# Kernel tuning notes

Measured on AMD Instinct MI355X. Metric: run time of the kernel, lower is better.

The kernel has to match this reference:

```python
import jax, jax.numpy as jnp
from jax import lax
import numpy as np

EPS = 1e-5

def _layer_norm(x):
    mu = jnp.mean(x, axis=-1, keepdims=True)
    var = jnp.mean(jnp.square(x - mu), axis=-1, keepdims=True)
    return (x - mu) / jnp.sqrt(var + EPS)

def setup_inputs() -> dict:
    key = jax.random.key(0)
    k1, k2 = jax.random.split(key)
    B, S, D = 2, 2048, 128
    n_hashes, num_buckets = 8, 32
    x = jax.random.normal(k1, (B, S, D), dtype=jnp.float32)
    input_mask = jnp.ones((B, S), dtype=jnp.float32)
    # random rotations for LSH hashing: (B, D, n_hashes, num_buckets//2)
    rotations = jax.random.normal(k2, (B, D, n_hashes, num_buckets // 2), dtype=jnp.float32)
    return {"x": x, "input_mask": input_mask, "rotations": rotations, "num_buckets": num_buckets}

def reference(x, input_mask, rotations, num_buckets):
    B, S, D = x.shape
    xn = _layer_norm(x)
    # LSH hashing: rotate, concat +/-, argmax over bucket axis -> (B, n_hashes, S)
    rot = jnp.einsum('bnd,bdhk->bhnk', xn, rotations)
    rot = jnp.concatenate([rot, -rot], axis=-1)
    buckets = jnp.argmax(rot, axis=-1)
    xm = xn * input_mask[..., None]
    # source loop reassigns round_buckets each hash round; only the last survives
    round_buckets = buckets[:, -1, :]  # (B, S)
    scale = 1.0 / jnp.sqrt(jnp.asarray(D, dtype=x.dtype))
    def body(out, bucket_id):
        m = (round_buckets == bucket_id).astype(xm.dtype)[..., None]  # (B,S,1)
        cb = xm * m  # zero out tokens outside the bucket (faithful to source)
        scores = jnp.einsum('bsd,btd->bst', cb, cb) * scale  # (B,S,S)
        attn = jax.nn.softmax(scores, axis=-1)
        out = out + jnp.einsum('bst,btd->bsd', attn, cb) * m
        return out, None
    out, _ = lax.scan(body, jnp.zeros_like(xm), jnp.arange(num_buckets))
    return out
```

## Files before the change

### kernel.cpp

```cpp
#include <hip/hip_runtime.h>
#include <math.h>

constexpr int B = 2;
constexpr int S = 2048;
constexpr int D = 128;
constexpr int NH = 8;
constexpr int NK = 16;
constexpr int NB = 32;
constexpr float EPS = 1e-5f;
constexpr float SCALE = 0.08838834764831845f;

constexpr int MAXN = 192;
constexpr int KP   = 136;
constexpr int TP   = 200;
constexpr int QSPLIT = 4;

typedef __attribute__((ext_vector_type(8))) short bf16x8;
typedef __attribute__((ext_vector_type(4))) float f32x4;

__device__ __forceinline__ ushort f2bf(float f) {
    uint u = __float_as_uint(f);
    u += 0x7FFFu + ((u >> 16) & 1u);
    return (ushort)(u >> 16);
}

__global__ __launch_bounds__(256) void ln_hash_kernel(
    const float* __restrict__ x, const float* __restrict__ mask,
    const float* __restrict__ rot, ushort* __restrict__ xmb,
    int* __restrict__ bucket, float* __restrict__ selfp)
{
    const int wave = threadIdx.x >> 6;
    const int lane = threadIdx.x & 63;
    const int row  = blockIdx.x * 4 + wave;
    const int b    = row >> 11;

    const float v0 = x[(size_t)row * D + lane];
    const float v1 = x[(size_t)row * D + lane + 64];

    float s = v0 + v1;
    #pragma unroll
    for (int off = 32; off > 0; off >>= 1) s += __shfl_xor(s, off, 64);
    const float mu = s * (1.0f / 128.0f);

    const float c0 = v0 - mu, c1 = v1 - mu;
    float s2 = c0 * c0 + c1 * c1;
    #pragma unroll
    for (int off = 32; off > 0; off >>= 1) s2 += __shfl_xor(s2, off, 64);
    const float rstd = 1.0f / sqrtf(s2 * (1.0f / 128.0f) + EPS);

    const float xn0 = c0 * rstd, xn1 = c1 * rstd;
    const float mk = mask[row];
    xmb[(size_t)row * D + lane]      = f2bf(xn0 * mk);
    xmb[(size_t)row * D + lane + 64] = f2bf(xn1 * mk);

    const float* r0 = rot + (((size_t)(b * D + lane)) * NH + (NH - 1)) * NK;
    const float* r1 = rot + (((size_t)(b * D + lane + 64)) * NH + (NH - 1)) * NK;
    float racc[NK];
    #pragma unroll
    for (int k = 0; k < NK; ++k) racc[k] = xn0 * r0[k] + xn1 * r1[k];
    #pragma unroll
    for (int k = 0; k < NK; ++k) {
        float t = racc[k];
        #pragma unroll
        for (int off = 32; off > 0; off >>= 1) t += __shfl_xor(t, off, 64);
        racc[k] = t;
    }

    float best = racc[0]; int bi = 0;
    #pragma unroll
    for (int k = 1; k < NK; ++k) if (racc[k] > best) { best = racc[k]; bi = k; }
    #pragma unroll
    for (int k = 0; k < NK; ++k) if (-racc[k] > best) { best = -racc[k]; bi = k + NK; }

    if (lane == 0) {
        bucket[row] = bi;
        selfp[row] = SCALE * s2 * rstd * rstd * mk * mk;
    }
}

__global__ __launch_bounds__(256) void attn_kernel(
    const ushort* __restrict__ xmb, const int* __restrict__ bucket,
    const float* __restrict__ selfp, float* __restrict__ out)
{
    const int bg   = blockIdx.x >> 2;
    const int qs   = blockIdx.x & 3;
    const int b    = bg >> 5;
    const int beta = bg & 31;
    const int tid  = threadIdx.x;
    const int lane = tid & 63;
    const int wave = tid >> 6;
    const int col  = lane & 15;
    const int quad = lane >> 4;

    __shared__ __align__(16) ushort Kb[MAXN * KP];
    __shared__ __align__(16) ushort KTb[D * TP];
    __shared__ __align__(16) float  w[16 * TP];
    __shared__ __align__(16) ushort Pt[16 * TP];
    __shared__ int   idx[MAXN];
    __shared__ float scratch[256];
    __shared__ float Mrow[16], invrow[16];
    __shared__ int   wsum[4];

    const int base = b * S;
    const int4* bp = (const int4*)(bucket + base);
    const int4 v0 = bp[tid * 2];
    const int4 v1 = bp[tid * 2 + 1];
    int m0 = (v0.x == beta) | ((v0.y == beta) << 1) | ((v0.z == beta) << 2) |
             ((v0.w == beta) << 3) | ((v1.x == beta) << 4) | ((v1.y == beta) << 5) |
             ((v1.z == beta) << 6) | ((v1.w == beta) << 7);
    const int cntl = __popc(m0);

    int inc = cntl;
    #pragma unroll
    for (int off = 1; off < 64; off <<= 1) {
        const int t = __shfl_up(inc, off, 64);
        if (lane >= off) inc += t;
    }
    if (lane == 63) wsum[wave] = inc;
    __syncthreads();
    int start = inc - cntl;
    #pragma unroll
    for (int wv = 0; wv < 4; ++wv) if (wv < wave) start += wsum[wv];
    const int ntot = wsum[0] + wsum[1] + wsum[2] + wsum[3];
    const int n = min(ntot, MAXN);

    {
        const int t0 = tid * 8;
        int p = start;
        #pragma unroll
        for (int k = 0; k < 8; ++k)
            if ((m0 >> k) & 1) { if (p < MAXN) idx[p] = t0 + k; ++p; }
    }
    __syncthreads();
    if (n == 0) return;
    const int npad32 = (n + 31) & ~31;

    for (int c = tid; c < n * 16; c += 256) {
        const int i = c >> 4, ch = c & 15;
        *(bf16x8*)&Kb[i * KP + ch * 8] =
            *(const bf16x8*)(xmb + (size_t)(base + idx[i]) * D + ch * 8);
    }
    __syncthreads();

    for (int e = tid; e < n * D; e += 256) {
        const int j = e >> 7, d = e & 127;
        KTb[d * TP + j] = Kb[j * KP + d];
    }
    for (int e = tid; e < D * 32; e += 256) {
        const int d = e >> 5, j = n + (e & 31);
        if (j < npad32) KTb[d * TP + j] = 0;
    }
    for (int e = tid; e < 16 * 32; e += 256) {
        const int r = e >> 5, j = n + (e & 31);
        if (j < npad32) Pt[r * TP + j] = 0;
    }
    __syncthreads();

    for (int qt = qs; qt * 16 < n; qt += QSPLIT) {
        const int q0 = qt * 16;
        const int rows = min(16, n - q0);

        for (int kt = wave; kt * 16 < n; kt += 4) {
            const int J0 = kt * 16;
            f32x4 acc = {0.f, 0.f, 0.f, 0.f};
            #pragma unroll
            for (int ks = 0; ks < 4; ++ks) {
                const bf16x8 a = *(const bf16x8*)&Kb[(q0 + col) * KP + quad * 8 + ks * 32];
                const bf16x8 bb = *(const bf16x8*)&Kb[(J0 + col) * KP + quad * 8 + ks * 32];
                acc = __builtin_amdgcn_mfma_f32_16x16x32_bf16(a, bb, acc, 0, 0, 0);
            }
            #pragma unroll
            for (int r = 0; r < 4; ++r)
                w[(quad * 4 + r) * TP + J0 + col] = acc[r] * SCALE;
        }
        __syncthreads();

        if (tid < rows)
            w[tid * TP + q0 + tid] = selfp[base + idx[q0 + tid]];
        __syncthreads();

        {
            const int r = tid >> 4, g = tid & 15;
            float pm = 0.0f;
            if (r < rows)
                for (int j = g; j < n; j += 16) pm = fmaxf(pm, w[r * TP + j]);
            scratch[tid] = pm;
            __syncthreads();
            if (tid < 16 && tid < rows) {
                float m = scratch[tid * 16];
                #pragma unroll
                for (int k = 1; k < 16; ++k) m = fmaxf(m, scratch[tid * 16 + k]);
                Mrow[tid] = m;
            }
            __syncthreads();
            float ps = 0.0f;
            if (r < rows) {
                const float M = Mrow[r];
                for (int j = g; j < n; j += 16) {
                    const float e = expf(w[r * TP + j] - M);
                    Pt[r * TP + j] = f2bf(e);
                    ps += e;
                }
            }
            scratch[tid] = ps;
            __syncthreads();
            if (tid < 16 && tid < rows) {
                float ssum = 0.0f;
                #pragma unroll
                for (int k = 0; k < 16; ++k) ssum += scratch[tid * 16 + k];
                ssum += (float)(S - n) * expf(-Mrow[tid]);
                invrow[tid] = 1.0f / ssum;
            }
            __syncthreads();
        }

        for (int dt = wave; dt < 8; dt += 4) {
            f32x4 acc = {0.f, 0.f, 0.f, 0.f};
            for (int ks = 0; ks < npad32 / 32; ++ks) {
                const bf16x8 a = *(const bf16x8*)&Pt[col * TP + ks * 32 + quad * 8];
                const bf16x8 bb = *(const bf16x8*)&KTb[(dt * 16 + col) * TP + ks * 32 + quad * 8];
                acc = __builtin_amdgcn_mfma_f32_16x16x32_bf16(a, bb, acc, 0, 0, 0);
            }
            #pragma unroll
            for (int r = 0; r < 4; ++r) {
                const int rr = quad * 4 + r;
                if (rr < rows)
                    out[(size_t)(base + idx[q0 + rr]) * D + dt * 16 + col] =
                        acc[r] * invrow[rr];
            }
        }
        __syncthreads();
    }
}

extern "C" void kernel_launch(void* const* d_in, const int* in_sizes, int n_in,
                              void* d_out, int out_size, void* d_ws, size_t ws_size,
                              hipStream_t stream) {
    const float* x    = (const float*)d_in[0];
    const float* mask = (const float*)d_in[1];
    const float* rot  = (const float*)d_in[2];

    char* ws = (char*)d_ws;
    ushort* xmb  = (ushort*)ws;                  ws += (size_t)B * S * D * sizeof(ushort);
    int*    bkt  = (int*)ws;                     ws += (size_t)B * S * sizeof(int);
    float*  self = (float*)ws;
    float*  out  = (float*)d_out;

    ln_hash_kernel<<<B * S / 4, 256, 0, stream>>>(x, mask, rot, xmb, bkt, self);
    attn_kernel<<<B * NB * QSPLIT, 256, 0, stream>>>(xmb, bkt, self, out);
}
```

Baseline: 79.11 us.

## Fuse LN-hash and bucket attention into one cooperative kernel with grid sync

Merges the layernorm/hash kernel and the attention kernel into a single cooperative launch of 256 blocks, where each block first normalizes and hashes 16 rows and then a grid-wide sync precedes the bucket attention. The transpose into KTb now happens during the gather, removing a pass and a barrier. The softmax row max and sum reductions use wave shuffles instead of shared scratch and several __syncthreads. This removes one kernel launch and some barriers, at the cost of a grid barrier and less parallelism in the hashing phase.

```diff
diff --git a/kernel.cpp b/kernel.cpp
--- a/kernel.cpp
+++ b/kernel.cpp
@@ -1,5 +1,8 @@
 #include <hip/hip_runtime.h>
+#include <hip/hip_cooperative_groups.h>
 #include <math.h>
+
+namespace cg = cooperative_groups;
 
 constexpr int B = 2;
 constexpr int S = 2048;
@@ -14,6 +17,7 @@
 constexpr int KP   = 136;
 constexpr int TP   = 200;
 constexpr int QSPLIT = 4;
+constexpr int GRID  = B * NB * QSPLIT;
 
 typedef __attribute__((ext_vector_type(8))) short bf16x8;
 typedef __attribute__((ext_vector_type(4))) float f32x4;
@@ -24,82 +28,80 @@
     return (ushort)(u >> 16);
 }
 
-__global__ __launch_bounds__(256) void ln_hash_kernel(
+__global__ __launch_bounds__(256) void fused_kernel(
     const float* __restrict__ x, const float* __restrict__ mask,
     const float* __restrict__ rot, ushort* __restrict__ xmb,
-    int* __restrict__ bucket, float* __restrict__ selfp)
+    int* __restrict__ bucket, float* __restrict__ selfp,
+    float* __restrict__ out)
 {
-    const int wave = threadIdx.x >> 6;
-    const int lane = threadIdx.x & 63;
-    const int row  = blockIdx.x * 4 + wave;
-    const int b    = row >> 11;
-
-    const float v0 = x[(size_t)row * D + lane];
-    const float v1 = x[(size_t)row * D + lane + 64];
-
-    float s = v0 + v1;
-    #pragma unroll
-    for (int off = 32; off > 0; off >>= 1) s += __shfl_xor(s, off, 64);
-    const float mu = s * (1.0f / 128.0f);
-
-    const float c0 = v0 - mu, c1 = v1 - mu;
-    float s2 = c0 * c0 + c1 * c1;
-    #pragma unroll
-    for (int off = 32; off > 0; off >>= 1) s2 += __shfl_xor(s2, off, 64);
-    const float rstd = 1.0f / sqrtf(s2 * (1.0f / 128.0f) + EPS);
-
-    const float xn0 = c0 * rstd, xn1 = c1 * rstd;
-    const float mk = mask[row];
-    xmb[(size_t)row * D + lane]      = f2bf(xn0 * mk);
-    xmb[(size_t)row * D + lane + 64] = f2bf(xn1 * mk);
-
-    const float* r0 = rot + (((size_t)(b * D + lane)) * NH + (NH - 1)) * NK;
-    const float* r1 = rot + (((size_t)(b * D + lane + 64)) * NH + (NH - 1)) * NK;
-    float racc[NK];
-    #pragma unroll
-    for (int k = 0; k < NK; ++k) racc[k] = xn0 * r0[k] + xn1 * r1[k];
-    #pragma unroll
-    for (int k = 0; k < NK; ++k) {
-        float t = racc[k];
-        #pragma unroll
-        for (int off = 32; off > 0; off >>= 1) t += __shfl_xor(t, off, 64);
-        racc[k] = t;
-    }
-
-    float best = racc[0]; int bi = 0;
-    #pragma unroll
-    for (int k = 1; k < NK; ++k) if (racc[k] > best) { best = racc[k]; bi = k; }
-    #pragma unroll
-    for (int k = 0; k < NK; ++k) if (-racc[k] > best) { best = -racc[k]; bi = k + NK; }
-
-    if (lane == 0) {
-        bucket[row] = bi;
-        selfp[row] = SCALE * s2 * rstd * rstd * mk * mk;
-    }
-}
-
-__global__ __launch_bounds__(256) void attn_kernel(
-    const ushort* __restrict__ xmb, const int* __restrict__ bucket,
-    const float* __restrict__ selfp, float* __restrict__ out)
-{
-    const int bg   = blockIdx.x >> 2;
-    const int qs   = blockIdx.x & 3;
-    const int b    = bg >> 5;
-    const int beta = bg & 31;
     const int tid  = threadIdx.x;
+    const int wave = tid >> 6;
     const int lane = tid & 63;
-    const int wave = tid >> 6;
-    const int col  = lane & 15;
-    const int quad = lane >> 4;
 
     __shared__ __align__(16) ushort Kb[MAXN * KP];
     __shared__ __align__(16) ushort KTb[D * TP];
     __shared__ __align__(16) float  w[16 * TP];
     __shared__ __align__(16) ushort Pt[16 * TP];
     __shared__ int   idx[MAXN];
-    __shared__ float scratch[256];
-    __shared__ float Mrow[16], invrow[16];
+    __shared__ float invrow[16];
     __shared__ int   wsum[4];
+
+    #pragma unroll
+    for (int i = 0; i < 4; ++i) {
+        const int row = blockIdx.x * 16 + wave * 4 + i;
+        const int b   = row >> 11;
+
+        const float2 v = *(const float2*)(x + (size_t)row * D + lane * 2);
+        float s = v.x + v.y;
+        #pragma unroll
+        for (int off = 32; off > 0; off >>= 1) s += __shfl_xor(s, off, 64);
+        const float mu = s * (1.0f / 128.0f);
+
+        const float c0 = v.x - mu, c1 = v.y - mu;
+        float s2 = c0 * c0 + c1 * c1;
+        #pragma unroll
+        for (int off = 32; off > 0; off >>= 1) s2 += __shfl_xor(s2, off, 64);
+        const float rstd = 1.0f / sqrtf(s2 * (1.0f / 128.0f) + EPS);
+
+        const float xn0 = c0 * rstd, xn1 = c1 * rstd;
+        const float mk = mask[row];
+        ushort2 pk;
+        pk.x = f2bf(xn0 * mk);
+        pk.y = f2bf(xn1 * mk);
+        *(ushort2*)(xmb + (size_t)row * D + lane * 2) = pk;
+
+        const float* rp = rot + (((size_t)(b * D + lane * 2)) * NH + (NH - 1)) * NK;
+        float racc[NK];
+        #pragma unroll
+        for (int k = 0; k < NK; ++k) racc[k] = xn0 * rp[k] + xn1 * rp[k + NH * NK];
+        #pragma unroll
+        for (int k = 0; k < NK; ++k) {
+            float t = racc[k];
+            #pragma unroll
+            for (int off = 32; off > 0; off >>= 1) t += __shfl_xor(t, off, 64);
+            racc[k] = t;
+        }
+
+        float best = racc[0]; int bi = 0;
+        #pragma unroll
+        for (int k = 1; k < NK; ++k) if (racc[k] > best) { best = racc[k]; bi = k; }
+        #pragma unroll
+        for (int k = 0; k < NK; ++k) if (-racc[k] > best) { best = -racc[k]; bi = k + NK; }
+
+        if (lane == 0) {
+            bucket[row] = bi;
+            selfp[row]  = SCALE * s2 * rstd * rstd * mk * mk;
+        }
+    }
+
+    cg::this_grid().sync();
+
+    const int bg   = blockIdx.x >> 2;
+    const int qs   = blockIdx.x & 3;
+    const int b    = bg >> 5;
+    const int beta = bg & 31;
+    const int col  = lane & 15;
+    const int quad = lane >> 4;
 
     const int base = b * S;
     const int4* bp = (const int4*)(bucket + base);
@@ -137,14 +139,11 @@
 
     for (int c = tid; c < n * 16; c += 256) {
         const int i = c >> 4, ch = c & 15;
-        *(bf16x8*)&Kb[i * KP + ch * 8] =
-            *(const bf16x8*)(xmb + (size_t)(base + idx[i]) * D + ch * 8);
-    }
-    __syncthreads();
-
-    for (int e = tid; e < n * D; e += 256) {
-        const int j = e >> 7, d = e & 127;
-        KTb[d * TP + j] = Kb[j * KP + d];
+        const bf16x8 v = *(const bf16x8*)(xmb + (size_t)(base + idx[i]) * D + ch * 8);
+        *(bf16x8*)&Kb[i * KP + ch * 8] = v;
+        #pragma unroll
+        for (int e = 0; e < 8; ++e)
+            KTb[(ch * 8 + e) * TP + i] = (ushort)v[e];
     }
     for (int e = tid; e < D * 32; e += 256) {
         const int d = e >> 5, j = n + (e & 31);
@@ -165,7 +164,7 @@
             f32x4 acc = {0.f, 0.f, 0.f, 0.f};
             #pragma unroll
             for (int ks = 0; ks < 4; ++ks) {
-                const bf16x8 a = *(const bf16x8*)&Kb[(q0 + col) * KP + quad * 8 + ks * 32];
+                const bf16x8 a  = *(const bf16x8*)&Kb[(q0 + col) * KP + quad * 8 + ks * 32];
                 const bf16x8 bb = *(const bf16x8*)&Kb[(J0 + col) * KP + quad * 8 + ks * 32];
                 acc = __builtin_amdgcn_mfma_f32_16x16x32_bf16(a, bb, acc, 0, 0, 0);
             }
@@ -175,49 +174,42 @@
         }
         __syncthreads();
 
-        if (tid < rows)
-            w[tid * TP + q0 + tid] = selfp[base + idx[q0 + tid]];
-        __syncthreads();
-
         {
-            const int r = tid >> 4, g = tid & 15;
+            const int r = wave * 4 + (lane >> 4);
+            const int g = lane & 15;
+            const bool act = r < rows;
+
+            if (act && g == ((q0 + r) & 15))
+                w[r * TP + q0 + r] = selfp[base + idx[q0 + r]];
+
             float pm = 0.0f;
-            if (r < rows)
+            if (act)
                 for (int j = g; j < n; j += 16) pm = fmaxf(pm, w[r * TP + j]);
-            scratch[tid] = pm;
-            __syncthreads();
-            if (tid < 16 && tid < rows) {
-                float m = scratch[tid * 16];
-                #pragma unroll
-                for (int k = 1; k < 16; ++k) m = fmaxf(m, scratch[tid * 16 + k]);
-                Mrow[tid] = m;
-            }
-            __syncthreads();
+            #pragma unroll
+            for (int off = 1; off < 16; off <<= 1)
+                pm = fmaxf(pm, __shfl_xor(pm, off, 64));
+            const float M = pm;
+
             float ps = 0.0f;
-            if (r < rows) {
-                const float M = Mrow[r];
+            if (act) {
                 for (int j = g; j < n; j += 16) {
                     const float e = expf(w[r * TP + j] - M);
                     Pt[r * TP + j] = f2bf(e);
                     ps += e;
                 }
             }
-            scratch[tid] = ps;
-            __syncthreads();
-            if (tid < 16 && tid < rows) {
-                float ssum = 0.0f;
-                #pragma unroll
-                for (int k = 0; k < 16; ++k) ssum += scratch[tid * 16 + k];
-                ssum += (float)(S - n) * expf(-Mrow[tid]);
-                invrow[tid] = 1.0f / ssum;
-            }
-            __syncthreads();
-        }
+            #pragma unroll
+            for (int off = 1; off < 16; off <<= 1)
+                ps += __shfl_xor(ps, off, 64);
+            if (act && g == 0)
+                invrow[r] = 1.0f / (ps + (float)(S - n) * expf(-M));
+        }
+        __syncthreads();
 
         for (int dt = wave; dt < 8; dt += 4) {
             f32x4 acc = {0.f, 0.f, 0.f, 0.f};
             for (int ks = 0; ks < npad32 / 32; ++ks) {
-                const bf16x8 a = *(const bf16x8*)&Pt[col * TP + ks * 32 + quad * 8];
+                const bf16x8 a  = *(const bf16x8*)&Pt[col * TP + ks * 32 + quad * 8];
                 const bf16x8 bb = *(const bf16x8*)&KTb[(dt * 16 + col) * TP + ks * 32 + quad * 8];
                 acc = __builtin_amdgcn_mfma_f32_16x16x32_bf16(a, bb, acc, 0, 0, 0);
             }
@@ -246,6 +238,8 @@
     float*  self = (float*)ws;
     float*  out  = (float*)d_out;
 
-    ln_hash_kernel<<<B * S / 4, 256, 0, stream>>>(x, mask, rot, xmb, bkt, self);
-    attn_kernel<<<B * NB * QSPLIT, 256, 0, stream>>>(xmb, bkt, self, out);
+    void* args[] = {(void*)&x, (void*)&mask, (void*)&rot,
+                    (void*)&xmb, (void*)&bkt, (void*)&self, (void*)&out};
+    hipLaunchCooperativeKernel((const void*)fused_kernel, dim3(GRID), dim3(256),
+                               args, 0, stream);
 }
```

Result: slower. 115.7 us (+46.3%).
